# Optimization experiments

Hardware: AMD Instinct MI355X
Metric: run time of the kernel (lower is better)

## Reference

```python
import jax, jax.numpy as jnp
import numpy as np

D = 384      # n_embed_dims
H = 6        # n_heads
HS = D // H  # head_size = 64
T = 256      # block_size
B = 256
EPS = 1e-5


def setup_inputs() -> dict:
    key = jax.random.key(0)
    ks = jax.random.split(key, 12)
    s_in = 1.0 / np.sqrt(D)
    s_ff = 1.0 / np.sqrt(4 * D)
    return {
        "x": jax.random.normal(ks[0], (B, T, D), jnp.float32),
        # per-head QKV weights, stacked [H, D, HS] (Linear bias=False)
        "wq": jax.random.normal(ks[1], (H, D, HS), jnp.float32) * s_in,
        "wk": jax.random.normal(ks[2], (H, D, HS), jnp.float32) * s_in,
        "wv": jax.random.normal(ks[3], (H, D, HS), jnp.float32) * s_in,
        "w_proj": jax.random.normal(ks[4], (D, D), jnp.float32) * s_in,
        "b_proj": jax.random.normal(ks[5], (D,), jnp.float32) * s_in,
        "w1": jax.random.normal(ks[6], (D, 4 * D), jnp.float32) * s_in,
        "b1": jax.random.normal(ks[7], (4 * D,), jnp.float32) * s_in,
        "w2": jax.random.normal(ks[8], (4 * D, D), jnp.float32) * s_ff,
        "b2": jax.random.normal(ks[9], (D,), jnp.float32) * s_ff,
        "g1": jnp.ones((D,), jnp.float32),
        "be1": jnp.zeros((D,), jnp.float32),
        "g2": jnp.ones((D,), jnp.float32),
        "be2": jnp.zeros((D,), jnp.float32),
    }


def _layernorm(x, g, b):
    mu = jnp.mean(x, axis=-1, keepdims=True)
    var = jnp.mean(jnp.square(x - mu), axis=-1, keepdims=True)
    return (x - mu) * jax.lax.rsqrt(var + EPS) * g + b


def _attention(x, wq, wk, wv, w_proj, b_proj):
    # faithful quirk: scale = 1/sqrt(C) with C = full embed dim (384)
    scale = 1.0 / jnp.sqrt(jnp.asarray(D, x.dtype))
    q = jnp.einsum("btd,hde->bhte", x, wq)  # [B,H,T,HS]
    k = jnp.einsum("btd,hde->bhte", x, wk)
    v = jnp.einsum("btd,hde->bhte", x, wv)
    w = jnp.einsum("bhte,bhse->bhts", q, k) * scale  # [B,H,T,T], no mask
    w = jax.nn.softmax(w, axis=-1)
    out = jnp.einsum("bhts,bhse->bhte", w, v)  # [B,H,T,HS]
    # concat heads along feature dim (head order matches torch cat)
    out = out.transpose(0, 2, 1, 3).reshape(x.shape[0], x.shape[1], D)
    return out @ w_proj + b_proj


def reference(x, wq, wk, wv, w_proj, b_proj, w1, b1, w2, b2, g1, be1, g2, be2):
    x = x + _attention(_layernorm(x, g1, be1), wq, wk, wv, w_proj, b_proj)
    h = _layernorm(x, g2, be2)
    h = jax.nn.relu(h @ w1 + b1) @ w2 + b2  # dropout = eval-mode identity
    return x + h
```

## Files before the change

### kernel.cpp

```cpp
#include <hip/hip_runtime.h>
#include <stdint.h>

#define NTOK 65536
#define DE 384
#define QSTR 1280

typedef __bf16 bf16x8 __attribute__((ext_vector_type(8)));
typedef float  f32x4  __attribute__((ext_vector_type(4)));
typedef float  f32x16 __attribute__((ext_vector_type(16)));
typedef unsigned short u16x8 __attribute__((ext_vector_type(8)));

__device__ __forceinline__ unsigned short f2bf(float f) {
  union { float fl; unsigned u; } a; a.fl = f;
  unsigned r = a.u + 0x7fffu + ((a.u >> 16) & 1u);
  return (unsigned short)(r >> 16);
}
__device__ __forceinline__ float b2f(unsigned short s) {
  union { unsigned u; float f; } v; v.u = (unsigned)s << 16; return v.f;
}

__device__ __forceinline__ void gll16(const void* g, void* l) {
  __builtin_amdgcn_global_load_lds((const __attribute__((address_space(1))) void*)g,
                                   (__attribute__((address_space(3))) void*)l, 16, 0, 0);
}

__device__ __forceinline__ bf16x8 ds128(unsigned addr) {
  bf16x8 r;
  asm volatile("ds_read_b128 %0, %1" : "=v"(r) : "v"(addr));
  return r;
}

__global__ void pack_t(unsigned short* __restrict__ dst, const float* __restrict__ src,
                       int R, int C) {
  int t = blockIdx.x * 256 + threadIdx.x;
  if (t >= R * C) return;
  int r = t / C, c = t - r * C;
  dst[(size_t)c * R + r] = f2bf(src[t]);
}

__global__ void qkv_pack(const float* __restrict__ wq, const float* __restrict__ wk,
                         const float* __restrict__ wv, unsigned short* __restrict__ dst) {
  int t = blockIdx.x * 256 + threadIdx.x;
  if (t >= QSTR * 384) return;
  int n = t / 384, k = t - n * 384;
  unsigned short v = 0;
  if (n < 1152) {
    int which = n / 384, r = n - which * 384;
    const float* src = which == 0 ? wq : (which == 1 ? wk : wv);
    int h = r >> 6, e = r & 63;
    v = f2bf(src[h * 24576 + k * 64 + e]);
  }
  dst[t] = v;
}

__global__ __launch_bounds__(256) void ln_kernel(const float* __restrict__ x,
                                                 const float* __restrict__ g,
                                                 const float* __restrict__ be,
                                                 unsigned short* __restrict__ out) {
  int wave = threadIdx.x >> 6, lane = threadIdx.x & 63;
  size_t row = (size_t)blockIdx.x * 4 + wave;
  const float* xr = x + row * DE;
  int c0 = lane * 2;
  float2 v0 = *(const float2*)(xr + c0);
  float2 v1 = *(const float2*)(xr + 128 + c0);
  float2 v2 = *(const float2*)(xr + 256 + c0);
  float s  = v0.x + v0.y + v1.x + v1.y + v2.x + v2.y;
  float ss = v0.x*v0.x + v0.y*v0.y + v1.x*v1.x + v1.y*v1.y + v2.x*v2.x + v2.y*v2.y;
#pragma unroll
  for (int m = 1; m < 64; m <<= 1) { s += __shfl_xor(s, m); ss += __shfl_xor(ss, m); }
  float mu = s * (1.0f / 384.0f);
  float rstd = rsqrtf(ss * (1.0f / 384.0f) - mu * mu + 1e-5f);
  unsigned short* orow = out + row * DE;
  {
    float a0 = (v0.x - mu) * rstd * g[c0] + be[c0];
    float a1 = (v0.y - mu) * rstd * g[c0 + 1] + be[c0 + 1];
    *(unsigned*)(orow + c0) = (unsigned)f2bf(a0) | ((unsigned)f2bf(a1) << 16);
  }
  {
    int c = c0 + 128;
    float a0 = (v1.x - mu) * rstd * g[c] + be[c];
    float a1 = (v1.y - mu) * rstd * g[c + 1] + be[c + 1];
    *(unsigned*)(orow + c) = (unsigned)f2bf(a0) | ((unsigned)f2bf(a1) << 16);
  }
  {
    int c = c0 + 256;
    float a0 = (v2.x - mu) * rstd * g[c] + be[c];
    float a1 = (v2.y - mu) * rstd * g[c + 1] + be[c + 1];
    *(unsigned*)(orow + c) = (unsigned)f2bf(a0) | ((unsigned)f2bf(a1) << 16);
  }
}

template<int EPI, int BM, int BN, int WM, int WN>
__device__ __forceinline__
void gemm_core(const unsigned short* __restrict__ A, const unsigned short* __restrict__ Bt,
               int M, int K, int Nst, int stride, int ntx,
               const float* __restrict__ bias, const float* __restrict__ residf,
               const unsigned short* __restrict__ residb,
               const float* __restrict__ g2, const float* __restrict__ be2,
               float* __restrict__ outf, unsigned short* __restrict__ outb,
               unsigned short* __restrict__ out2) {
  constexpr int T = WM * WN * 64;
  constexpr int MWT = BM / WM, NWT = BN / WN;
  constexpr int MT = MWT / 32, NT = NWT / 32;
  constexpr int LA = (BM * 128) / (T * 16);
  constexpr int LB = (BN * 128) / (T * 16);
  __shared__ __align__(16) unsigned short As[2][BM * 64];
  __shared__ __align__(16) unsigned short Bs[2][BN * 64];
  __shared__ float red[(EPI == 1) ? BM : 1][4][2];
  const int tid = threadIdx.x;
  const int wave = tid >> 6, lane = tid & 63;

  const int nwg = gridDim.x;
  const int cpx = nwg >> 3;
  const int wg = (blockIdx.x & 7) * cpx + (blockIdx.x >> 3);
  const int bx = wg % ntx, by = wg / ntx;
  const int mBase = by * BM, nBase = bx * BN;
  const int wmi = wave / WN, wni = wave % WN;
  const int wm = wmi * MWT, wn = wni * NWT;
  const int cr = lane & 31;
  const int hg = lane >> 5;

  const unsigned asb = (unsigned)(uintptr_t)&As[0][0];
  const unsigned bsb = (unsigned)(uintptr_t)&Bs[0][0];

  f32x16 acc[MT][NT];
#pragma unroll
  for (int i = 0; i < MT; ++i)
#pragma unroll
    for (int j = 0; j < NT; ++j)
#pragma unroll
      for (int r = 0; r < 16; ++r) acc[i][j][r] = 0.f;

  auto stage = [&](int buf, int kt) {
#pragma unroll
    for (int i = 0; i < LA; ++i) {
      int Lb = i * (T * 16) + wave * 1024;
      int L = Lb + lane * 16;
      int row = L >> 7;
      int col = ((((L >> 4) & 7) ^ (row & 7) ^ ((row >> 3) & 3)) << 3);
      gll16(A + (size_t)(mBase + row) * K + kt + col, (unsigned short*)As[buf] + (Lb >> 1));
    }
#pragma unroll
    for (int i = 0; i < LB; ++i) {
      int Lb = i * (T * 16) + wave * 1024;
      int L = Lb + lane * 16;
      int row = L >> 7;
      int col = ((((L >> 4) & 7) ^ (row & 7) ^ ((row >> 3) & 3)) << 3);
      gll16(Bt + (size_t)(nBase + row) * K + kt + col, (unsigned short*)Bs[buf] + (Lb >> 1));
    }
  };

  const int NK = K >> 6;
  stage(0, 0);
  for (int t = 0; t < NK; ++t) {
    const int cur = t & 1;
    if (t + 1 < NK) {
      stage(cur ^ 1, (t + 1) << 6);
      if constexpr (LA + LB == 8)      asm volatile("s_waitcnt vmcnt(8)" ::: "memory");
      else if constexpr (LA + LB == 7) asm volatile("s_waitcnt vmcnt(7)" ::: "memory");
      else                             asm volatile("s_waitcnt vmcnt(6)" ::: "memory");
    } else {
      asm volatile("s_waitcnt vmcnt(0)" ::: "memory");
    }
    asm volatile("" ::: "memory");
    __builtin_amdgcn_s_barrier();
    asm volatile("" ::: "memory");

    const unsigned ab = asb + (cur ? (unsigned)(BM * 128) : 0u);
    const unsigned bb = bsb + (cur ? (unsigned)(BN * 128) : 0u);
#pragma unroll
    for (int k2 = 0; k2 < 2; ++k2) {
      bf16x8 bfr[2][NT], af[2][MT];
#pragma unroll
      for (int kk = 0; kk < 2; ++kk) {
        const int ks = k2 * 2 + kk;
#pragma unroll
        for (int nt = 0; nt < NT; ++nt) {
          int row = wn + nt * 32 + cr;
          unsigned slot = (unsigned)(((ks * 2 + hg) ^ (row & 7) ^ ((row >> 3) & 3)) & 7);
          bfr[kk][nt] = ds128(bb + (unsigned)(row << 7) + (slot << 4));
        }
#pragma unroll
        for (int mt = 0; mt < MT; ++mt) {
          int row = wm + mt * 32 + cr;
          unsigned slot = (unsigned)(((ks * 2 + hg) ^ (row & 7) ^ ((row >> 3) & 3)) & 7);
          af[kk][mt] = ds128(ab + (unsigned)(row << 7) + (slot << 4));
        }
      }
      asm volatile("s_waitcnt lgkmcnt(0)" ::: "memory");
      __builtin_amdgcn_sched_barrier(0);
      __builtin_amdgcn_s_setprio(1);
#pragma unroll
      for (int kk = 0; kk < 2; ++kk)
#pragma unroll
        for (int mt = 0; mt < MT; ++mt)
#pragma unroll
          for (int nt = 0; nt < NT; ++nt)
            acc[mt][nt] = __builtin_amdgcn_mfma_f32_32x32x16_bf16(af[kk][mt], bfr[kk][nt],
                                                                  acc[mt][nt], 0, 0, 0);
      __builtin_amdgcn_s_setprio(0);
    }
    asm volatile("" ::: "memory");
    __builtin_amdgcn_s_barrier();
    asm volatile("" ::: "memory");
  }

  if (EPI == 1) {
#pragma unroll
    for (int mt = 0; mt < MT; ++mt) {
#pragma unroll
      for (int nt = 0; nt < NT; ++nt) {
        const int gn = nBase + wn + nt * 32 + cr;
#pragma unroll
        for (int r = 0; r < 16; ++r) {
          const int gm = mBase + wm + mt * 32 + (r & 3) + ((r >> 2) << 3) + (hg << 2);
          size_t idx = (size_t)gm * stride + gn;
          acc[mt][nt][r] = acc[mt][nt][r] + bias[gn] + residf[idx];
        }
      }
    }
#pragma unroll
    for (int mt = 0; mt < MT; ++mt) {
#pragma unroll
      for (int r = 0; r < 16; ++r) {
        float s = 0.f, ss = 0.f;
#pragma unroll
        for (int nt = 0; nt < NT; ++nt) {
          float v = acc[mt][nt][r];
          s += v; ss += v * v;
        }
        s += __shfl_xor(s, 1);  ss += __shfl_xor(ss, 1);
        s += __shfl_xor(s, 2);  ss += __shfl_xor(ss, 2);
        s += __shfl_xor(s, 4);  ss += __shfl_xor(ss, 4);
        s += __shfl_xor(s, 8);  ss += __shfl_xor(ss, 8);
        s += __shfl_xor(s, 16); ss += __shfl_xor(ss, 16);
        if (cr == 0) {
          int row = wm + mt * 32 + (r & 3) + ((r >> 2) << 3) + (hg << 2);
          red[row][wni][0] = s;
          red[row][wni][1] = ss;
        }
      }
    }
    __syncthreads();
#pragma unroll
    for (int mt = 0; mt < MT; ++mt) {
#pragma unroll
      for (int r = 0; r < 16; ++r) {
        int row = wm + mt * 32 + (r & 3) + ((r >> 2) << 3) + (hg << 2);
        float s = red[row][0][0] + red[row][1][0] + red[row][2][0] + red[row][3][0];
        float ss = red[row][0][1] + red[row][1][1] + red[row][2][1] + red[row][3][1];
        float mu = s * (1.0f / 384.0f);
        float rstd = rsqrtf(ss * (1.0f / 384.0f) - mu * mu + 1e-5f);
        const int gm = mBase + row;
#pragma unroll
        for (int nt = 0; nt < NT; ++nt) {
          const int gn = nBase + wn + nt * 32 + cr;
          size_t idx = (size_t)gm * stride + gn;
          float x1v = acc[mt][nt][r];
          outb[idx] = f2bf(x1v);
          out2[idx] = f2bf((x1v - mu) * rstd * g2[gn] + be2[gn]);
        }
      }
    }
    return;
  }

#pragma unroll
  for (int mt = 0; mt < MT; ++mt) {
#pragma unroll
    for (int nt = 0; nt < NT; ++nt) {
      const int gn = nBase + wn + nt * 32 + cr;
      if (gn < Nst) {
#pragma unroll
        for (int r = 0; r < 16; ++r) {
          const int gm = mBase + wm + mt * 32 + (r & 3) + ((r >> 2) << 3) + (hg << 2);
          float val = acc[mt][nt][r];
          size_t idx = (size_t)gm * stride + gn;
          if (EPI == 0) {
            outb[idx] = f2bf(val);
          } else if (EPI == 2) {
            float rr = val + bias[gn];
            outb[idx] = f2bf(rr > 0.f ? rr : 0.f);
          } else {
            outf[idx] = val + bias[gn] + b2f(residb[idx]);
          }
        }
      }
    }
  }
}

__global__ __launch_bounds__(512, 1)
void gemm_qkv(const unsigned short* __restrict__ A, const unsigned short* __restrict__ Bt,
              int M, int K, int Nst, int stride, int ntx,
              const float* __restrict__ bias, const float* __restrict__ residf,
              const unsigned short* __restrict__ residb, float* __restrict__ outf,
              unsigned short* __restrict__ outb) {
  gemm_core<0, 256, 192, 4, 2>(A, Bt, M, K, Nst, stride, ntx, bias, residf, residb,
                               nullptr, nullptr, outf, outb, nullptr);
}
__global__ __launch_bounds__(512, 1)
void gemm_projln(const unsigned short* __restrict__ A, const unsigned short* __restrict__ Bt,
                 int M, int K, int Nst, int stride, int ntx,
                 const float* __restrict__ bias, const float* __restrict__ residf,
                 const float* __restrict__ g2, const float* __restrict__ be2,
                 unsigned short* __restrict__ outb, unsigned short* __restrict__ out2) {
  gemm_core<1, 128, 384, 2, 4>(A, Bt, M, K, Nst, stride, ntx, bias, residf, nullptr,
                               g2, be2, nullptr, outb, out2);
}
__global__ __launch_bounds__(512, 1)
void gemm_mlp1(const unsigned short* __restrict__ A, const unsigned short* __restrict__ Bt,
               int M, int K, int Nst, int stride, int ntx,
               const float* __restrict__ bias, const float* __restrict__ residf,
               const unsigned short* __restrict__ residb, float* __restrict__ outf,
               unsigned short* __restrict__ outb) {
  gemm_core<2, 256, 256, 2, 4>(A, Bt, M, K, Nst, stride, ntx, bias, residf, residb,
                               nullptr, nullptr, outf, outb, nullptr);
}
__global__ __launch_bounds__(512, 1)
void gemm_mlp2(const unsigned short* __restrict__ A, const unsigned short* __restrict__ Bt,
               int M, int K, int Nst, int stride, int ntx,
               const float* __restrict__ bias, const float* __restrict__ residf,
               const unsigned short* __restrict__ residb, float* __restrict__ outf,
               unsigned short* __restrict__ outb) {
  gemm_core<3, 256, 128, 4, 2>(A, Bt, M, K, Nst, stride, ntx, bias, residf, residb,
                               nullptr, nullptr, outf, outb, nullptr);
}

__global__ __launch_bounds__(256)
void attn_kernel(const unsigned short* __restrict__ qkvn, unsigned short* __restrict__ o) {
  __shared__ unsigned short Vt[64 * 256];
  __shared__ unsigned short Pw[4][64 * 32];
  const int bh = blockIdx.x;
  const int b = bh / 6, h = bh - b * 6;
  const unsigned short* base = qkvn + (size_t)(b * 256) * QSTR;
  const unsigned short* qb = base + h * 64;
  const unsigned short* kbp = base + 384 + h * 64;
  const unsigned short* vbp = base + 768 + h * 64;
  const int wave = threadIdx.x >> 6, lane = threadIdx.x & 63;
  const int fr = lane & 15, fg = lane >> 4;
  const int fk = fg << 3;
  const int qrow0 = wave << 6;
  const float scale = 0.051031036307982884f;
  const f32x4 z = {0.f, 0.f, 0.f, 0.f};

  {
    const int s = threadIdx.x;
    u16x8 v8[8];
#pragma unroll
    for (int j = 0; j < 8; ++j)
      v8[j] = *(const u16x8*)(vbp + (size_t)s * QSTR + j * 8);
#pragma unroll
    for (int e = 0; e < 64; ++e)
      Vt[(e << 8) + (s ^ ((e & 7) << 3))] = v8[e >> 3][e & 7];
  }
  __syncthreads();

  bf16x8 qf[4][2];
#pragma unroll
  for (int rb = 0; rb < 4; ++rb)
#pragma unroll
    for (int ks = 0; ks < 2; ++ks)
      qf[rb][ks] = *(const bf16x8*)(qb + (size_t)(qrow0 + rb * 16 + fr) * QSTR + ks * 32 + fk);

  f32x4 oacc[4][4];
  float psum[4][4];
#pragma unroll
  for (int rb = 0; rb < 4; ++rb)
#pragma unroll
    for (int nb = 0; nb < 4; ++nb) oacc[rb][nb] = z;
#pragma unroll
  for (int rb = 0; rb < 4; ++rb)
#pragma unroll
    for (int i = 0; i < 4; ++i) psum[rb][i] = 0.f;

  for (int kb2 = 0; kb2 < 8; ++kb2) {
#pragma unroll
    for (int c2 = 0; c2 < 2; ++c2) {
      int cb = kb2 * 2 + c2;
      bf16x8 kf0 = *(const bf16x8*)(kbp + (size_t)(cb * 16 + fr) * QSTR + fk);
      bf16x8 kf1 = *(const bf16x8*)(kbp + (size_t)(cb * 16 + fr) * QSTR + 32 + fk);
#pragma unroll
      for (int rb = 0; rb < 4; ++rb) {
        f32x4 s = __builtin_amdgcn_mfma_f32_16x16x32_bf16(qf[rb][0], kf0, z, 0, 0, 0);
        s = __builtin_amdgcn_mfma_f32_16x16x32_bf16(qf[rb][1], kf1, s, 0, 0, 0);
#pragma unroll
        for (int i = 0; i < 4; ++i) {
          float p = __expf(fminf(scale * s[i], 60.f));
          psum[rb][i] += p;
          Pw[wave][(rb * 16 + (fg << 2) + i) * 32 + c2 * 16 + fr] = f2bf(p);
        }
      }
    }
    bf16x8 pa[4], vf[4];
#pragma unroll
    for (int rb = 0; rb < 4; ++rb) pa[rb] = *(const bf16x8*)(&Pw[wave][(rb * 16 + fr) * 32 + fk]);
#pragma unroll
    for (int nb = 0; nb < 4; ++nb) {
      int e = nb * 16 + fr;
      vf[nb] = *(const bf16x8*)(&Vt[(e << 8) + ((kb2 * 32 + fk) ^ ((e & 7) << 3))]);
    }
#pragma unroll
    for (int rb = 0; rb < 4; ++rb)
#pragma unroll
      for (int nb = 0; nb < 4; ++nb)
        oacc[rb][nb] = __builtin_amdgcn_mfma_f32_16x16x32_bf16(pa[rb], vf[nb], oacc[rb][nb], 0, 0, 0);
  }

  float rs[4][4];
#pragma unroll
  for (int rb = 0; rb < 4; ++rb)
#pragma unroll
    for (int i = 0; i < 4; ++i) {
      float v = psum[rb][i];
      v += __shfl_xor(v, 1);
      v += __shfl_xor(v, 2);
      v += __shfl_xor(v, 4);
      v += __shfl_xor(v, 8);
      rs[rb][i] = 1.0f / v;
    }

#pragma unroll
  for (int rb = 0; rb < 4; ++rb)
#pragma unroll
    for (int nb = 0; nb < 4; ++nb)
#pragma unroll
      for (int i = 0; i < 4; ++i) {
        int token = b * 256 + qrow0 + rb * 16 + (fg << 2) + i;
        int gcol = h * 64 + nb * 16 + fr;
        o[(size_t)token * DE + gcol] = f2bf(oacc[rb][nb][i] * rs[rb][i]);
      }
}

extern "C" void kernel_launch(void* const* d_in, const int* in_sizes, int n_in,
                              void* d_out, int out_size, void* d_ws, size_t ws_size,
                              hipStream_t stream) {
  const float* x     = (const float*)d_in[0];
  const float* wq    = (const float*)d_in[1];
  const float* wk    = (const float*)d_in[2];
  const float* wv    = (const float*)d_in[3];
  const float* wproj = (const float*)d_in[4];
  const float* bproj = (const float*)d_in[5];
  const float* w1    = (const float*)d_in[6];
  const float* b1    = (const float*)d_in[7];
  const float* w2    = (const float*)d_in[8];
  const float* b2    = (const float*)d_in[9];
  const float* g1    = (const float*)d_in[10];
  const float* be1   = (const float*)d_in[11];
  const float* g2    = (const float*)d_in[12];
  const float* be2   = (const float*)d_in[13];

  char* ws = (char*)d_ws;
  unsigned short* xln   = (unsigned short*)(ws + 0);
  unsigned short* x1b   = (unsigned short*)(ws + 0);
  unsigned short* qkvn  = (unsigned short*)(ws + 50331648);
  unsigned short* hbuf  = (unsigned short*)(ws + 100663296);
  unsigned short* act   = (unsigned short*)(ws + 150994944);
  unsigned short* attno = (unsigned short*)(ws + 218103808);
  unsigned short* wqkvt = (unsigned short*)(ws + 352321536);
  unsigned short* wprjt = (unsigned short*)(ws + 352321536 + 983040);
  unsigned short* w1t   = (unsigned short*)(ws + 352321536 + 983040 + 294912);
  unsigned short* w2t   = (unsigned short*)(ws + 352321536 + 983040 + 294912 + 1179648);

  qkv_pack<<<(QSTR * 384 + 255) / 256, 256, 0, stream>>>(wq, wk, wv, wqkvt);
  pack_t<<<(147456 + 255) / 256, 256, 0, stream>>>(wprjt, wproj, 384, 384);
  pack_t<<<(589824 + 255) / 256, 256, 0, stream>>>(w1t, w1, 384, 1536);
  pack_t<<<(589824 + 255) / 256, 256, 0, stream>>>(w2t, w2, 1536, 384);

  ln_kernel<<<NTOK / 4, 256, 0, stream>>>(x, g1, be1, xln);

  gemm_qkv<<<6 * 256, 512, 0, stream>>>(xln, wqkvt, NTOK, 384, 1152, 1280, 6,
                                        nullptr, nullptr, nullptr, nullptr, qkvn);

  attn_kernel<<<1536, 256, 0, stream>>>(qkvn, attno);

  gemm_projln<<<512, 512, 0, stream>>>(attno, wprjt, NTOK, 384, 384, 384, 1,
                                       bproj, x, g2, be2, x1b, hbuf);

  gemm_mlp1<<<6 * 256, 512, 0, stream>>>(hbuf, w1t, NTOK, 384, 1536, 1536, 6,
                                         b1, nullptr, nullptr, nullptr, act);

  gemm_mlp2<<<3 * 256, 512, 0, stream>>>(act, w2t, NTOK, 1536, 384, 384, 3,
                                         b2, nullptr, x1b, (float*)d_out, nullptr);
}
```

Baseline: 516.6 us.

## Fuse attention with output projection, residual and LayerNorm2 in one kernel

Attention and the projection GEMM with its bias+residual+LayerNorm epilogue are merged into a single kernel. Each 512-thread workgroup handles 128 query tokens across all 6 heads and keeps the attention output in LDS, then runs the 384x384 projection against wprjt tiles streamed into LDS. This removes the global write and re-read of the attention output and one kernel launch. In exchange each workgroup now loops over heads serially with only 16 query rows per wave, runs just 512 workgroups, holds a large LDS footprint, and recomputes or reloads K and V per query half. Workspace buffers are also re-laid out so the MLP activation reuses the qkv region.

New measurement: 566.3 us. 9.6% more time.

```diff
diff --git a/kernel.cpp b/kernel.cpp
--- a/kernel.cpp
+++ b/kernel.cpp
@@ -94,11 +94,8 @@
 __device__ __forceinline__
 void gemm_core(const unsigned short* __restrict__ A, const unsigned short* __restrict__ Bt,
                int M, int K, int Nst, int stride, int ntx,
-               const float* __restrict__ bias, const float* __restrict__ residf,
-               const unsigned short* __restrict__ residb,
-               const float* __restrict__ g2, const float* __restrict__ be2,
-               float* __restrict__ outf, unsigned short* __restrict__ outb,
-               unsigned short* __restrict__ out2) {
+               const float* __restrict__ bias, const unsigned short* __restrict__ residb,
+               float* __restrict__ outf, unsigned short* __restrict__ outb) {
   constexpr int T = WM * WN * 64;
   constexpr int MWT = BM / WM, NWT = BN / WN;
   constexpr int MT = MWT / 32, NT = NWT / 32;
@@ -106,7 +103,6 @@
   constexpr int LB = (BN * 128) / (T * 16);
   __shared__ __align__(16) unsigned short As[2][BM * 64];
   __shared__ __align__(16) unsigned short Bs[2][BN * 64];
-  __shared__ float red[(EPI == 1) ? BM : 1][4][2];
   const int tid = threadIdx.x;
   const int wave = tid >> 6, lane = tid & 63;
 
@@ -115,8 +111,7 @@
   const int wg = (blockIdx.x & 7) * cpx + (blockIdx.x >> 3);
   const int bx = wg % ntx, by = wg / ntx;
   const int mBase = by * BM, nBase = bx * BN;
-  const int wmi = wave / WN, wni = wave % WN;
-  const int wm = wmi * MWT, wn = wni * NWT;
+  const int wm = (wave / WN) * MWT, wn = (wave % WN) * NWT;
   const int cr = lane & 31;
   const int hg = lane >> 5;
 
@@ -203,66 +198,6 @@
     asm volatile("" ::: "memory");
     __builtin_amdgcn_s_barrier();
     asm volatile("" ::: "memory");
-  }
-
-  if (EPI == 1) {
-#pragma unroll
-    for (int mt = 0; mt < MT; ++mt) {
-#pragma unroll
-      for (int nt = 0; nt < NT; ++nt) {
-        const int gn = nBase + wn + nt * 32 + cr;
-#pragma unroll
-        for (int r = 0; r < 16; ++r) {
-          const int gm = mBase + wm + mt * 32 + (r & 3) + ((r >> 2) << 3) + (hg << 2);
-          size_t idx = (size_t)gm * stride + gn;
-          acc[mt][nt][r] = acc[mt][nt][r] + bias[gn] + residf[idx];
-        }
-      }
-    }
-#pragma unroll
-    for (int mt = 0; mt < MT; ++mt) {
-#pragma unroll
-      for (int r = 0; r < 16; ++r) {
-        float s = 0.f, ss = 0.f;
-#pragma unroll
-        for (int nt = 0; nt < NT; ++nt) {
-          float v = acc[mt][nt][r];
-          s += v; ss += v * v;
-        }
-        s += __shfl_xor(s, 1);  ss += __shfl_xor(ss, 1);
-        s += __shfl_xor(s, 2);  ss += __shfl_xor(ss, 2);
-        s += __shfl_xor(s, 4);  ss += __shfl_xor(ss, 4);
-        s += __shfl_xor(s, 8);  ss += __shfl_xor(ss, 8);
-        s += __shfl_xor(s, 16); ss += __shfl_xor(ss, 16);
-        if (cr == 0) {
-          int row = wm + mt * 32 + (r & 3) + ((r >> 2) << 3) + (hg << 2);
-          red[row][wni][0] = s;
-          red[row][wni][1] = ss;
-        }
-      }
-    }
-    __syncthreads();
-#pragma unroll
-    for (int mt = 0; mt < MT; ++mt) {
-#pragma unroll
-      for (int r = 0; r < 16; ++r) {
-        int row = wm + mt * 32 + (r & 3) + ((r >> 2) << 3) + (hg << 2);
-        float s = red[row][0][0] + red[row][1][0] + red[row][2][0] + red[row][3][0];
-        float ss = red[row][0][1] + red[row][1][1] + red[row][2][1] + red[row][3][1];
-        float mu = s * (1.0f / 384.0f);
-        float rstd = rsqrtf(ss * (1.0f / 384.0f) - mu * mu + 1e-5f);
-        const int gm = mBase + row;
-#pragma unroll
-        for (int nt = 0; nt < NT; ++nt) {
-          const int gn = nBase + wn + nt * 32 + cr;
-          size_t idx = (size_t)gm * stride + gn;
-          float x1v = acc[mt][nt][r];
-          outb[idx] = f2bf(x1v);
-          out2[idx] = f2bf((x1v - mu) * rstd * g2[gn] + be2[gn]);
-        }
-      }
-    }
-    return;
   }
 
 #pragma unroll
@@ -292,144 +227,244 @@
 
 __global__ __launch_bounds__(512, 1)
 void gemm_qkv(const unsigned short* __restrict__ A, const unsigned short* __restrict__ Bt,
-              int M, int K, int Nst, int stride, int ntx,
-              const float* __restrict__ bias, const float* __restrict__ residf,
+              int M, int K, int Nst, int stride, int ntx, const float* __restrict__ bias,
               const unsigned short* __restrict__ residb, float* __restrict__ outf,
               unsigned short* __restrict__ outb) {
-  gemm_core<0, 256, 192, 4, 2>(A, Bt, M, K, Nst, stride, ntx, bias, residf, residb,
-                               nullptr, nullptr, outf, outb, nullptr);
-}
-__global__ __launch_bounds__(512, 1)
-void gemm_projln(const unsigned short* __restrict__ A, const unsigned short* __restrict__ Bt,
-                 int M, int K, int Nst, int stride, int ntx,
-                 const float* __restrict__ bias, const float* __restrict__ residf,
-                 const float* __restrict__ g2, const float* __restrict__ be2,
-                 unsigned short* __restrict__ outb, unsigned short* __restrict__ out2) {
-  gemm_core<1, 128, 384, 2, 4>(A, Bt, M, K, Nst, stride, ntx, bias, residf, nullptr,
-                               g2, be2, nullptr, outb, out2);
+  gemm_core<0, 256, 192, 4, 2>(A, Bt, M, K, Nst, stride, ntx, bias, residb, outf, outb);
 }
 __global__ __launch_bounds__(512, 1)
 void gemm_mlp1(const unsigned short* __restrict__ A, const unsigned short* __restrict__ Bt,
-               int M, int K, int Nst, int stride, int ntx,
-               const float* __restrict__ bias, const float* __restrict__ residf,
+               int M, int K, int Nst, int stride, int ntx, const float* __restrict__ bias,
                const unsigned short* __restrict__ residb, float* __restrict__ outf,
                unsigned short* __restrict__ outb) {
-  gemm_core<2, 256, 256, 2, 4>(A, Bt, M, K, Nst, stride, ntx, bias, residf, residb,
-                               nullptr, nullptr, outf, outb, nullptr);
+  gemm_core<2, 256, 256, 2, 4>(A, Bt, M, K, Nst, stride, ntx, bias, residb, outf, outb);
 }
 __global__ __launch_bounds__(512, 1)
 void gemm_mlp2(const unsigned short* __restrict__ A, const unsigned short* __restrict__ Bt,
-               int M, int K, int Nst, int stride, int ntx,
-               const float* __restrict__ bias, const float* __restrict__ residf,
+               int M, int K, int Nst, int stride, int ntx, const float* __restrict__ bias,
                const unsigned short* __restrict__ residb, float* __restrict__ outf,
                unsigned short* __restrict__ outb) {
-  gemm_core<3, 256, 128, 4, 2>(A, Bt, M, K, Nst, stride, ntx, bias, residf, residb,
-                               nullptr, nullptr, outf, outb, nullptr);
-}
-
-__global__ __launch_bounds__(256)
-void attn_kernel(const unsigned short* __restrict__ qkvn, unsigned short* __restrict__ o) {
-  __shared__ unsigned short Vt[64 * 256];
-  __shared__ unsigned short Pw[4][64 * 32];
-  const int bh = blockIdx.x;
-  const int b = bh / 6, h = bh - b * 6;
-  const unsigned short* base = qkvn + (size_t)(b * 256) * QSTR;
-  const unsigned short* qb = base + h * 64;
-  const unsigned short* kbp = base + 384 + h * 64;
-  const unsigned short* vbp = base + 768 + h * 64;
-  const int wave = threadIdx.x >> 6, lane = threadIdx.x & 63;
-  const int fr = lane & 15, fg = lane >> 4;
-  const int fk = fg << 3;
-  const int qrow0 = wave << 6;
+  gemm_core<3, 256, 128, 4, 2>(A, Bt, M, K, Nst, stride, ntx, bias, residb, outf, outb);
+}
+
+__global__ __launch_bounds__(512)
+void attnproj(const unsigned short* __restrict__ qkvn, const unsigned short* __restrict__ wprjt,
+              const float* __restrict__ bproj, const float* __restrict__ x,
+              const float* __restrict__ g2, const float* __restrict__ be2,
+              unsigned short* __restrict__ x1b, unsigned short* __restrict__ hbuf) {
+  __shared__ __align__(16) unsigned short AO[48 * 1032];
+  __shared__ __align__(16) unsigned short SCR[24576];
+  __shared__ float red[128][4][2];
+
+  const int tid = threadIdx.x;
+  const int wave = tid >> 6, lane = tid & 63;
+  const int wg = blockIdx.x;
+  const size_t tok0 = (size_t)wg << 7;
+  const unsigned short* base = qkvn + (size_t)(wg >> 1) * 256 * QSTR;
+  const int q0 = (wg & 1) << 7;
+
+  unsigned short* Vt = SCR;
+  unsigned short* Pww = SCR + 16384 + wave * 512;
+  const unsigned aob = (unsigned)(uintptr_t)&AO[0];
+  const unsigned bsb = (unsigned)(uintptr_t)&SCR[0];
+
+  const int fr = lane & 15, fg = lane >> 4, fk = fg << 3;
   const float scale = 0.051031036307982884f;
   const f32x4 z = {0.f, 0.f, 0.f, 0.f};
 
-  {
-    const int s = threadIdx.x;
-    u16x8 v8[8];
-#pragma unroll
-    for (int j = 0; j < 8; ++j)
-      v8[j] = *(const u16x8*)(vbp + (size_t)s * QSTR + j * 8);
-#pragma unroll
-    for (int e = 0; e < 64; ++e)
-      Vt[(e << 8) + (s ^ ((e & 7) << 3))] = v8[e >> 3][e & 7];
-  }
-  __syncthreads();
-
-  bf16x8 qf[4][2];
-#pragma unroll
-  for (int rb = 0; rb < 4; ++rb)
-#pragma unroll
-    for (int ks = 0; ks < 2; ++ks)
-      qf[rb][ks] = *(const bf16x8*)(qb + (size_t)(qrow0 + rb * 16 + fr) * QSTR + ks * 32 + fk);
-
-  f32x4 oacc[4][4];
-  float psum[4][4];
-#pragma unroll
-  for (int rb = 0; rb < 4; ++rb)
-#pragma unroll
-    for (int nb = 0; nb < 4; ++nb) oacc[rb][nb] = z;
-#pragma unroll
-  for (int rb = 0; rb < 4; ++rb)
-#pragma unroll
-    for (int i = 0; i < 4; ++i) psum[rb][i] = 0.f;
-
-  for (int kb2 = 0; kb2 < 8; ++kb2) {
-#pragma unroll
-    for (int c2 = 0; c2 < 2; ++c2) {
-      int cb = kb2 * 2 + c2;
-      bf16x8 kf0 = *(const bf16x8*)(kbp + (size_t)(cb * 16 + fr) * QSTR + fk);
-      bf16x8 kf1 = *(const bf16x8*)(kbp + (size_t)(cb * 16 + fr) * QSTR + 32 + fk);
-#pragma unroll
-      for (int rb = 0; rb < 4; ++rb) {
-        f32x4 s = __builtin_amdgcn_mfma_f32_16x16x32_bf16(qf[rb][0], kf0, z, 0, 0, 0);
-        s = __builtin_amdgcn_mfma_f32_16x16x32_bf16(qf[rb][1], kf1, s, 0, 0, 0);
+  for (int h = 0; h < 6; ++h) {
+    const unsigned short* qb  = base + h * 64;
+    const unsigned short* kbp = base + 384 + h * 64;
+    const unsigned short* vbp = base + 768 + h * 64;
+    {
+      int s = tid & 255, half = tid >> 8;
+      u16x8 v8[4];
+#pragma unroll
+      for (int j = 0; j < 4; ++j)
+        v8[j] = *(const u16x8*)(vbp + (size_t)s * QSTR + half * 32 + j * 8);
+#pragma unroll
+      for (int e2 = 0; e2 < 32; ++e2) {
+        int e = half * 32 + e2;
+        Vt[(e << 8) + (s ^ ((e & 7) << 3))] = v8[e2 >> 3][e2 & 7];
+      }
+    }
+    __syncthreads();
+
+    bf16x8 qf0 = *(const bf16x8*)(qb + (size_t)(q0 + wave * 16 + fr) * QSTR + fk);
+    bf16x8 qf1 = *(const bf16x8*)(qb + (size_t)(q0 + wave * 16 + fr) * QSTR + 32 + fk);
+
+    f32x4 oacc[4];
+    float psum[4];
+#pragma unroll
+    for (int nb = 0; nb < 4; ++nb) oacc[nb] = z;
+#pragma unroll
+    for (int i = 0; i < 4; ++i) psum[i] = 0.f;
+
+    for (int kb2 = 0; kb2 < 8; ++kb2) {
+#pragma unroll
+      for (int c2 = 0; c2 < 2; ++c2) {
+        int cb = kb2 * 2 + c2;
+        bf16x8 kf0 = *(const bf16x8*)(kbp + (size_t)(cb * 16 + fr) * QSTR + fk);
+        bf16x8 kf1 = *(const bf16x8*)(kbp + (size_t)(cb * 16 + fr) * QSTR + 32 + fk);
+        f32x4 s = __builtin_amdgcn_mfma_f32_16x16x32_bf16(qf0, kf0, z, 0, 0, 0);
+        s = __builtin_amdgcn_mfma_f32_16x16x32_bf16(qf1, kf1, s, 0, 0, 0);
 #pragma unroll
         for (int i = 0; i < 4; ++i) {
           float p = __expf(fminf(scale * s[i], 60.f));
-          psum[rb][i] += p;
-          Pw[wave][(rb * 16 + (fg << 2) + i) * 32 + c2 * 16 + fr] = f2bf(p);
+          psum[i] += p;
+          Pww[((fg << 2) + i) * 32 + c2 * 16 + fr] = f2bf(p);
         }
       }
-    }
-    bf16x8 pa[4], vf[4];
-#pragma unroll
-    for (int rb = 0; rb < 4; ++rb) pa[rb] = *(const bf16x8*)(&Pw[wave][(rb * 16 + fr) * 32 + fk]);
-#pragma unroll
-    for (int nb = 0; nb < 4; ++nb) {
-      int e = nb * 16 + fr;
-      vf[nb] = *(const bf16x8*)(&Vt[(e << 8) + ((kb2 * 32 + fk) ^ ((e & 7) << 3))]);
-    }
-#pragma unroll
-    for (int rb = 0; rb < 4; ++rb)
+      bf16x8 pa = *(const bf16x8*)(Pww + fr * 32 + fk);
+      bf16x8 vf[4];
+#pragma unroll
+      for (int nb = 0; nb < 4; ++nb) {
+        int e = nb * 16 + fr;
+        vf[nb] = *(const bf16x8*)(&Vt[(e << 8) + ((kb2 * 32 + fk) ^ ((e & 7) << 3))]);
+      }
 #pragma unroll
       for (int nb = 0; nb < 4; ++nb)
-        oacc[rb][nb] = __builtin_amdgcn_mfma_f32_16x16x32_bf16(pa[rb], vf[nb], oacc[rb][nb], 0, 0, 0);
-  }
-
-  float rs[4][4];
-#pragma unroll
-  for (int rb = 0; rb < 4; ++rb)
+        oacc[nb] = __builtin_amdgcn_mfma_f32_16x16x32_bf16(pa, vf[nb], oacc[nb], 0, 0, 0);
+    }
+
+    float rs[4];
 #pragma unroll
     for (int i = 0; i < 4; ++i) {
-      float v = psum[rb][i];
+      float v = psum[i];
       v += __shfl_xor(v, 1);
       v += __shfl_xor(v, 2);
       v += __shfl_xor(v, 4);
       v += __shfl_xor(v, 8);
-      rs[rb][i] = 1.0f / v;
-    }
-
-#pragma unroll
-  for (int rb = 0; rb < 4; ++rb)
-#pragma unroll
-    for (int nb = 0; nb < 4; ++nb)
+      rs[i] = 1.0f / v;
+    }
+
+#pragma unroll
+    for (int nb = 0; nb < 4; ++nb) {
 #pragma unroll
       for (int i = 0; i < 4; ++i) {
-        int token = b * 256 + qrow0 + rb * 16 + (fg << 2) + i;
-        int gcol = h * 64 + nb * 16 + fr;
-        o[(size_t)token * DE + gcol] = f2bf(oacc[rb][nb][i] * rs[rb][i]);
-      }
+        int tr = wave * 16 + (fg << 2) + i;
+        int c = h * 64 + nb * 16 + fr;
+        AO[(c >> 3) * 1032 + tr * 8 + (c & 7)] = f2bf(oacc[nb][i] * rs[i]);
+      }
+    }
+    __syncthreads();
+  }
+
+  const int cr = lane & 31, hg = lane >> 5;
+  const int wm = (wave >> 2) << 6;
+  const int wni = wave & 3;
+  const int wn = wni * 96;
+
+  f32x16 acc[2][3];
+#pragma unroll
+  for (int mt = 0; mt < 2; ++mt)
+#pragma unroll
+    for (int nt = 0; nt < 3; ++nt)
+#pragma unroll
+      for (int r = 0; r < 16; ++r) acc[mt][nt][r] = 0.f;
+
+  for (int t = 0; t < 6; ++t) {
+#pragma unroll
+    for (int i = 0; i < 6; ++i) {
+      int Lb = i * 8192 + wave * 1024;
+      int L = Lb + lane * 16;
+      int row = L >> 7;
+      int col = ((((L >> 4) & 7) ^ (row & 7) ^ ((row >> 3) & 3)) << 3);
+      gll16(wprjt + (size_t)row * 384 + t * 64 + col, SCR + (Lb >> 1));
+    }
+    asm volatile("s_waitcnt vmcnt(0)" ::: "memory");
+    __builtin_amdgcn_s_barrier();
+    asm volatile("" ::: "memory");
+
+#pragma unroll
+    for (int k2 = 0; k2 < 2; ++k2) {
+      bf16x8 bfr[2][3], af[2][2];
+#pragma unroll
+      for (int kk = 0; kk < 2; ++kk) {
+        const int sl = (k2 * 2 + kk) * 2 + hg;
+#pragma unroll
+        for (int nt = 0; nt < 3; ++nt) {
+          int row = wn + nt * 32 + cr;
+          unsigned slot = (unsigned)((sl ^ (row & 7) ^ ((row >> 3) & 3)) & 7);
+          bfr[kk][nt] = ds128(bsb + (unsigned)(row << 7) + (slot << 4));
+        }
+        const int sa = t * 8 + sl;
+#pragma unroll
+        for (int mt = 0; mt < 2; ++mt) {
+          int row = wm + mt * 32 + cr;
+          af[kk][mt] = ds128(aob + (unsigned)sa * 2064u + (unsigned)(row << 4));
+        }
+      }
+      asm volatile("s_waitcnt lgkmcnt(0)" ::: "memory");
+      __builtin_amdgcn_sched_barrier(0);
+      __builtin_amdgcn_s_setprio(1);
+#pragma unroll
+      for (int kk = 0; kk < 2; ++kk)
+#pragma unroll
+        for (int mt = 0; mt < 2; ++mt)
+#pragma unroll
+          for (int nt = 0; nt < 3; ++nt)
+            acc[mt][nt] = __builtin_amdgcn_mfma_f32_32x32x16_bf16(af[kk][mt], bfr[kk][nt],
+                                                                  acc[mt][nt], 0, 0, 0);
+      __builtin_amdgcn_s_setprio(0);
+    }
+    asm volatile("" ::: "memory");
+    __builtin_amdgcn_s_barrier();
+    asm volatile("" ::: "memory");
+  }
+
+#pragma unroll
+  for (int mt = 0; mt < 2; ++mt)
+#pragma unroll
+    for (int nt = 0; nt < 3; ++nt) {
+      const int gn = wn + nt * 32 + cr;
+#pragma unroll
+      for (int r = 0; r < 16; ++r) {
+        const int lr = wm + mt * 32 + (r & 3) + ((r >> 2) << 3) + (hg << 2);
+        size_t idx = (tok0 + lr) * DE + gn;
+        acc[mt][nt][r] = acc[mt][nt][r] + bproj[gn] + x[idx];
+      }
+    }
+#pragma unroll
+  for (int mt = 0; mt < 2; ++mt)
+#pragma unroll
+    for (int r = 0; r < 16; ++r) {
+      float s = 0.f, ss = 0.f;
+#pragma unroll
+      for (int nt = 0; nt < 3; ++nt) {
+        float v = acc[mt][nt][r];
+        s += v; ss += v * v;
+      }
+      s += __shfl_xor(s, 1);  ss += __shfl_xor(ss, 1);
+      s += __shfl_xor(s, 2);  ss += __shfl_xor(ss, 2);
+      s += __shfl_xor(s, 4);  ss += __shfl_xor(ss, 4);
+      s += __shfl_xor(s, 8);  ss += __shfl_xor(ss, 8);
+      s += __shfl_xor(s, 16); ss += __shfl_xor(ss, 16);
+      if (cr == 0) {
+        int row = wm + mt * 32 + (r & 3) + ((r >> 2) << 3) + (hg << 2);
+        red[row][wni][0] = s;
+        red[row][wni][1] = ss;
+      }
+    }
+  __syncthreads();
+#pragma unroll
+  for (int mt = 0; mt < 2; ++mt)
+#pragma unroll
+    for (int r = 0; r < 16; ++r) {
+      int row = wm + mt * 32 + (r & 3) + ((r >> 2) << 3) + (hg << 2);
+      float s = red[row][0][0] + red[row][1][0] + red[row][2][0] + red[row][3][0];
+      float ss = red[row][0][1] + red[row][1][1] + red[row][2][1] + red[row][3][1];
+      float mu = s * (1.0f / 384.0f);
+      float rstd = rsqrtf(ss * (1.0f / 384.0f) - mu * mu + 1e-5f);
+#pragma unroll
+      for (int nt = 0; nt < 3; ++nt) {
+        const int gn = wn + nt * 32 + cr;
+        size_t idx = (tok0 + row) * DE + gn;
+        float x1v = acc[mt][nt][r];
+        x1b[idx] = f2bf(x1v);
+        hbuf[idx] = f2bf((x1v - mu) * rstd * g2[gn] + be2[gn]);
+      }
+    }
 }
 
 extern "C" void kernel_launch(void* const* d_in, const int* in_sizes, int n_in,
@@ -454,13 +489,12 @@
   unsigned short* xln   = (unsigned short*)(ws + 0);
   unsigned short* x1b   = (unsigned short*)(ws + 0);
   unsigned short* qkvn  = (unsigned short*)(ws + 50331648);
-  unsigned short* hbuf  = (unsigned short*)(ws + 100663296);
-  unsigned short* act   = (unsigned short*)(ws + 150994944);
-  unsigned short* attno = (unsigned short*)(ws + 218103808);
-  unsigned short* wqkvt = (unsigned short*)(ws + 352321536);
-  unsigned short* wprjt = (unsigned short*)(ws + 352321536 + 983040);
-  unsigned short* w1t   = (unsigned short*)(ws + 352321536 + 983040 + 294912);
-  unsigned short* w2t   = (unsigned short*)(ws + 352321536 + 983040 + 294912 + 1179648);
+  unsigned short* act   = (unsigned short*)(ws + 50331648);
+  unsigned short* hbuf  = (unsigned short*)(ws + 251658240);
+  unsigned short* wqkvt = (unsigned short*)(ws + 301989888);
+  unsigned short* wprjt = (unsigned short*)(ws + 301989888 + 983040);
+  unsigned short* w1t   = (unsigned short*)(ws + 301989888 + 983040 + 294912);
+  unsigned short* w2t   = (unsigned short*)(ws + 301989888 + 983040 + 294912 + 1179648);
 
   qkv_pack<<<(QSTR * 384 + 255) / 256, 256, 0, stream>>>(wq, wk, wv, wqkvt);
   pack_t<<<(147456 + 255) / 256, 256, 0, stream>>>(wprjt, wproj, 384, 384);
@@ -470,16 +504,13 @@
   ln_kernel<<<NTOK / 4, 256, 0, stream>>>(x, g1, be1, xln);
 
   gemm_qkv<<<6 * 256, 512, 0, stream>>>(xln, wqkvt, NTOK, 384, 1152, 1280, 6,
-                                        nullptr, nullptr, nullptr, nullptr, qkvn);
-
-  attn_kernel<<<1536, 256, 0, stream>>>(qkvn, attno);
-
-  gemm_projln<<<512, 512, 0, stream>>>(attno, wprjt, NTOK, 384, 384, 384, 1,
-                                       bproj, x, g2, be2, x1b, hbuf);
+                                        nullptr, nullptr, nullptr, qkvn);
+
+  attnproj<<<512, 512, 0, stream>>>(qkvn, wprjt, bproj, x, g2, be2, x1b, hbuf);
 
   gemm_mlp1<<<6 * 256, 512, 0, stream>>>(hbuf, w1t, NTOK, 384, 1536, 1536, 6,
-                                         b1, nullptr, nullptr, nullptr, act);
+                                         b1, nullptr, nullptr, act);
 
   gemm_mlp2<<<3 * 256, 512, 0, stream>>>(act, w2t, NTOK, 1536, 384, 384, 3,
-                                         b2, nullptr, x1b, (float*)d_out, nullptr);
-}
+                                         b2, x1b, (float*)d_out, nullptr);
+}
```
